# Kernel optimization log

Hardware: AMD Instinct MI355X
Metric: run time of the kernel (lower is better)

The kernel has to match this reference:

```python
import jax, jax.numpy as jnp
import numpy as np

D_MODEL = 512
NUM_HEADS = 8
HEAD_DIM = D_MODEL // NUM_HEADS
MAX_REL = 2


def setup_inputs() -> dict:
    key = jax.random.key(0)
    ks = jax.random.split(key, 12)
    B, S = 2, 4096
    std = 1.0 / np.sqrt(D_MODEL)
    inp = {
        'q': jax.random.normal(ks[0], (B, S, D_MODEL), jnp.float32),
        'k': jax.random.normal(ks[1], (B, S, D_MODEL), jnp.float32),
        'v': jax.random.normal(ks[2], (B, S, D_MODEL), jnp.float32),
        'Wq': jax.random.normal(ks[3], (D_MODEL, D_MODEL), jnp.float32) * std,
        'bq': jnp.zeros((D_MODEL,), jnp.float32),
        'Wk': jax.random.normal(ks[4], (D_MODEL, D_MODEL), jnp.float32) * std,
        'bk': jnp.zeros((D_MODEL,), jnp.float32),
        'Wv': jax.random.normal(ks[5], (D_MODEL, D_MODEL), jnp.float32) * std,
        'bv': jnp.zeros((D_MODEL,), jnp.float32),
        'Wo': jax.random.normal(ks[6], (D_MODEL, D_MODEL), jnp.float32) * std,
        'bo': jnp.zeros((D_MODEL,), jnp.float32),
        'rel_pos': jax.random.normal(ks[7], (NUM_HEADS, 2 * MAX_REL + 1), jnp.float32),
    }
    return inp


def _rel_bias(rel_pos, seq_len):
    pos = jnp.arange(seq_len)
    rel = pos[None, :] - pos[:, None]              # [S,S]
    idx = jnp.clip(rel, -MAX_REL, MAX_REL) + MAX_REL
    return rel_pos[:, idx]                         # [H,S,S]


def reference(q, k, v, Wq, bq, Wk, bk, Wv, bv, Wo, bo, rel_pos):
    B, S, D = q.shape
    H, Hd = NUM_HEADS, HEAD_DIM
    # torch Linear: x @ W.T + b
    Q = (q @ Wq.T + bq).reshape(B, S, H, Hd).transpose(0, 2, 1, 3)  # [B,H,S,Hd]
    K = (k @ Wk.T + bk).reshape(B, S, H, Hd).transpose(0, 2, 1, 3)
    V = (v @ Wv.T + bv).reshape(B, S, H, Hd).transpose(0, 2, 1, 3)
    scores = jnp.einsum('bhqd,bhkd->bhqk', Q, K) / jnp.sqrt(jnp.float32(Hd))
    scores = scores + _rel_bias(rel_pos, S)[None]                  # [B,H,S,S]
    probs = jax.nn.softmax(scores, axis=-1)
    attn = jnp.einsum('bhqk,bhkd->bhqd', probs, V)                 # [B,H,S,Hd]
    attn = attn.transpose(0, 2, 1, 3).reshape(B, S, D)
    return attn @ Wo.T + bo
```

## Files before the change

### kernel.cpp

```cpp
#include <hip/hip_runtime.h>

typedef __bf16 bf16_t;
typedef __bf16 bf16x4 __attribute__((ext_vector_type(4)));
typedef __bf16 bf16x8 __attribute__((ext_vector_type(8)));
typedef float f32x4 __attribute__((ext_vector_type(4)));

#define MFMA16(a, b, c) __builtin_amdgcn_mfma_f32_16x16x32_bf16(a, b, c, 0, 0, 0)
#define LOG2E 1.4426950408889634f
#define SHIFT 16.0f

#define GLL(g, l)                                                      \
  __builtin_amdgcn_global_load_lds(                                    \
      (const __attribute__((address_space(1))) void*)(g),              \
      (__attribute__((address_space(3))) void*)(l), 16, 0, 0)

static constexpr int NB = 2;
static constexpr int SEQ = 4096;
static constexpr int DM = 512;
static constexpr int NH = 8;
static constexpr int HD = 64;
static constexpr int M_ROWS = NB * SEQ;

__global__ __launch_bounds__(256) void cvt_w_kernel(
    const float* __restrict__ w0, const float* __restrict__ w1,
    const float* __restrict__ w2, const float* __restrict__ w3,
    bf16_t* __restrict__ out) {
  const float* src = (blockIdx.y == 0) ? w0 : (blockIdx.y == 1) ? w1
                   : (blockIdx.y == 2) ? w2 : w3;
  int i = (blockIdx.x * 256 + threadIdx.x) * 4;
  float4 v = *(const float4*)(src + i);
  bf16_t* o = out + blockIdx.y * (DM * DM) + i;
  o[0] = (bf16_t)v.x; o[1] = (bf16_t)v.y; o[2] = (bf16_t)v.z; o[3] = (bf16_t)v.w;
}

template <int XMODE>
__device__ __forceinline__ void gemm_body64(
    const void* __restrict__ Xv, const bf16_t* __restrict__ Wm,
    const float* __restrict__ bias, void* __restrict__ Out,
    int omode, float scale) {
  __shared__ bf16_t Asm[2][64 * 64];
  __shared__ bf16_t Bsm[2][128 * 64];

  const int tid = threadIdx.x;
  const int w = tid >> 6;
  const int lane = tid & 63;
  const int quad = lane >> 4, l15 = lane & 15;
  const int l8 = lane >> 3;
  const int swcol = ((lane & 7) ^ (l8 & 7)) * 8;
  const int m0 = blockIdx.x * 64;
  const int n0 = blockIdx.y * 128;
  const int moff = (w & 1) * 32;
  const int noff = (w >> 1) * 64;

  const bf16_t* Xb = (const bf16_t*)Xv;
  const float* Xf = (const float*)Xv;

  const int arow = tid >> 2;
  const int aseg = (tid & 3) * 16;
  const int ach = (tid & 3) * 2;
  const int asw = arow & 7;

  f32x4 acc[2][4];
#pragma unroll
  for (int mb = 0; mb < 2; mb++)
#pragma unroll
    for (int nb = 0; nb < 4; nb++) { acc[mb][nb][0] = 0.f; acc[mb][nb][1] = 0.f; acc[mb][nb][2] = 0.f; acc[mb][nb][3] = 0.f; }

#pragma unroll
  for (int j = 0; j < 4; j++) {
    const int row = j * 32 + w * 8 + l8;
    GLL(Wm + (size_t)(n0 + row) * DM + swcol, &Bsm[0][(j * 256 + w * 64) * 8]);
  }
  if (XMODE == 1) {
#pragma unroll
    for (int j = 0; j < 2; j++) {
      const int row = j * 32 + w * 8 + l8;
      GLL(Xb + (size_t)(m0 + row) * DM + swcol, &Asm[0][(j * 256 + w * 64) * 8]);
    }
  } else {
    const float* src = Xf + (size_t)(m0 + arow) * DM + aseg;
    float4 x0 = *(const float4*)(src);
    float4 x1 = *(const float4*)(src + 4);
    float4 x2 = *(const float4*)(src + 8);
    float4 x3 = *(const float4*)(src + 12);
    bf16x8 p0, p1;
    p0[0] = (bf16_t)x0.x; p0[1] = (bf16_t)x0.y; p0[2] = (bf16_t)x0.z; p0[3] = (bf16_t)x0.w;
    p0[4] = (bf16_t)x1.x; p0[5] = (bf16_t)x1.y; p0[6] = (bf16_t)x1.z; p0[7] = (bf16_t)x1.w;
    p1[0] = (bf16_t)x2.x; p1[1] = (bf16_t)x2.y; p1[2] = (bf16_t)x2.z; p1[3] = (bf16_t)x2.w;
    p1[4] = (bf16_t)x3.x; p1[5] = (bf16_t)x3.y; p1[6] = (bf16_t)x3.z; p1[7] = (bf16_t)x3.w;
    *(bf16x8*)&Asm[0][arow * 64 + ((ach ^ asw) * 8)] = p0;
    *(bf16x8*)&Asm[0][arow * 64 + (((ach + 1) ^ asw) * 8)] = p1;
  }
  __syncthreads();

  for (int ks = 0; ks < 8; ks++) {
    const int p = ks & 1, pn = p ^ 1;
    float4 xr0, xr1, xr2, xr3;
    if (ks < 7) {
      const int k0n = (ks + 1) * 64;
      if (XMODE == 0) {
        const float* src = Xf + (size_t)(m0 + arow) * DM + k0n + aseg;
        xr0 = *(const float4*)(src);
        xr1 = *(const float4*)(src + 4);
        xr2 = *(const float4*)(src + 8);
        xr3 = *(const float4*)(src + 12);
      } else {
#pragma unroll
        for (int j = 0; j < 2; j++) {
          const int row = j * 32 + w * 8 + l8;
          GLL(Xb + (size_t)(m0 + row) * DM + k0n + swcol,
              &Asm[pn][(j * 256 + w * 64) * 8]);
        }
      }
#pragma unroll
      for (int j = 0; j < 4; j++) {
        const int row = j * 32 + w * 8 + l8;
        GLL(Wm + (size_t)(n0 + row) * DM + k0n + swcol,
            &Bsm[pn][(j * 256 + w * 64) * 8]);
      }
    }

#pragma unroll
    for (int kd = 0; kd < 2; kd++) {
      const int fch = (((kd << 2) + quad) ^ (l15 & 7)) << 3;
      bf16x8 bfr[4];
#pragma unroll
      for (int nb = 0; nb < 4; nb++)
        bfr[nb] = *(const bf16x8*)&Bsm[p][(noff + nb * 16 + l15) * 64 + fch];
#pragma unroll
      for (int mb = 0; mb < 2; mb++) {
        bf16x8 a = *(const bf16x8*)&Asm[p][(moff + mb * 16 + l15) * 64 + fch];
#pragma unroll
        for (int nb = 0; nb < 4; nb++) acc[mb][nb] = MFMA16(a, bfr[nb], acc[mb][nb]);
      }
    }

    if (XMODE == 0 && ks < 7) {
      bf16x8 p0, p1;
      p0[0] = (bf16_t)xr0.x; p0[1] = (bf16_t)xr0.y; p0[2] = (bf16_t)xr0.z; p0[3] = (bf16_t)xr0.w;
      p0[4] = (bf16_t)xr1.x; p0[5] = (bf16_t)xr1.y; p0[6] = (bf16_t)xr1.z; p0[7] = (bf16_t)xr1.w;
      p1[0] = (bf16_t)xr2.x; p1[1] = (bf16_t)xr2.y; p1[2] = (bf16_t)xr2.z; p1[3] = (bf16_t)xr2.w;
      p1[4] = (bf16_t)xr3.x; p1[5] = (bf16_t)xr3.y; p1[6] = (bf16_t)xr3.z; p1[7] = (bf16_t)xr3.w;
      *(bf16x8*)&Asm[pn][arow * 64 + ((ach ^ asw) * 8)] = p0;
      *(bf16x8*)&Asm[pn][arow * 64 + (((ach + 1) ^ asw) * 8)] = p1;
    }
    __syncthreads();
  }

#pragma unroll
  for (int nb = 0; nb < 4; nb++) {
    const int n = n0 + noff + nb * 16 + l15;
    const float bn = bias[n];
    const int h = n >> 6, dd = n & 63;
#pragma unroll
    for (int mb = 0; mb < 2; mb++) {
      const int mbase = m0 + moff + mb * 16 + quad * 4;
      const int bb = mbase >> 12, s = mbase & 4095;
      if (omode == 0) {
#pragma unroll
        for (int r = 0; r < 4; r++) {
          const float val = (acc[mb][nb][r] + bn) * scale;
          ((bf16_t*)Out)[(size_t)((bb * NH + h) * SEQ + s + r) * HD + dd] = (bf16_t)val;
        }
      } else if (omode == 1) {
        bf16x4 pk;
#pragma unroll
        for (int r = 0; r < 4; r++) pk[r] = (bf16_t)(acc[mb][nb][r] + bn);
        *(bf16x4*)&((bf16_t*)Out)[(((size_t)(bb * NH + h) * HD + dd) << 12) + s] = pk;
      } else {
#pragma unroll
        for (int r = 0; r < 4; r++)
          ((float*)Out)[(size_t)(mbase + r) * DM + n] = acc[mb][nb][r] + bn;
      }
    }
  }
}

__global__ __launch_bounds__(256, 3) void qkv_kernel(
    const float* __restrict__ q, const float* __restrict__ k,
    const float* __restrict__ v, const bf16_t* __restrict__ Wall,
    const float* __restrict__ bq, const float* __restrict__ bk,
    const float* __restrict__ bv, bf16_t* __restrict__ Qb,
    bf16_t* __restrict__ Kb, bf16_t* __restrict__ Vb, float qscale) {
  const int z = blockIdx.z;
  const float* X = (z == 0) ? q : (z == 1) ? k : v;
  const float* bias = (z == 0) ? bq : (z == 1) ? bk : bv;
  bf16_t* Out = (z == 0) ? Qb : (z == 1) ? Kb : Vb;
  gemm_body64<0>(X, Wall + (size_t)z * DM * DM, bias, Out,
                 (z == 2) ? 1 : 0, (z == 0) ? qscale : 1.0f);
}

__global__ __launch_bounds__(256, 3) void oproj_kernel(
    const bf16_t* __restrict__ X, const bf16_t* __restrict__ Wm,
    const float* __restrict__ bias, float* __restrict__ Out) {
  gemm_body64<1>(X, Wm, bias, Out, 2, 1.0f);
}

__global__ __launch_bounds__(256, 2) void attn_kernel(
    const bf16_t* __restrict__ Qb, const bf16_t* __restrict__ Kb,
    const bf16_t* __restrict__ Vb, const float* __restrict__ rel_pos,
    bf16_t* __restrict__ attn_out) {
  __shared__ bf16_t Kt[2][64 * 64];
  __shared__ bf16_t Vt[2][64 * 64];
  __shared__ bf16_t Pt[4][32 * 64];

  const int tid = threadIdx.x;
  const int w = tid >> 6;
  const int lane = tid & 63;
  const int quad = lane >> 4, l15 = lane & 15;
  const int bh = blockIdx.y;
  const int b = bh >> 3, h = bh & 7;
  const int qlo = blockIdx.x * 128 + w * 32;

  const float rb0 = rel_pos[h * 5 + 0] * LOG2E;
  const float rb1 = rel_pos[h * 5 + 1] * LOG2E;
  const float rb2 = rel_pos[h * 5 + 2] * LOG2E;
  const float rb3 = rel_pos[h * 5 + 3] * LOG2E;
  const float rb4 = rel_pos[h * 5 + 4] * LOG2E;

  bf16x8 qf[2][2];
#pragma unroll
  for (int mb = 0; mb < 2; mb++)
#pragma unroll
    for (int kd = 0; kd < 2; kd++)
      qf[mb][kd] = *(const bf16x8*)(Qb + (size_t)(bh * SEQ + qlo + mb * 16 + l15) * HD + kd * 32 + 8 * quad);

  f32x4 o[2][4];
#pragma unroll
  for (int mb = 0; mb < 2; mb++)
#pragma unroll
    for (int db = 0; db < 4; db++) { o[mb][db][0] = 0.f; o[mb][db][1] = 0.f; o[mb][db][2] = 0.f; o[mb][db][3] = 0.f; }
  f32x4 l4[2];
  l4[0][0] = 0.f; l4[0][1] = 0.f; l4[0][2] = 0.f; l4[0][3] = 0.f;
  l4[1][0] = 0.f; l4[1][1] = 0.f; l4[1][2] = 0.f; l4[1][3] = 0.f;

  bf16x8 ones;
#pragma unroll
  for (int i = 0; i < 8; i++) ones[i] = (bf16_t)1.0f;

  const int srow = (w << 4) + (lane >> 3);
  const int scol = (((lane & 7) ^ (lane >> 3)) << 3);
  const bf16_t* kg0 = Kb + ((size_t)(bh * SEQ + srow) << 6) + scol;
  const bf16_t* vg0 = Vb + (((size_t)(bh * HD + srow)) << 12) + scol;
  const int ldst = (w << 10);

  const int sw = l15 & 7;
  const int kfo0 = (l15 << 6) + ((quad ^ sw) << 3);
  const int kfo1 = (l15 << 6) + (((quad + 4) ^ sw) << 3);

  GLL(kg0, &Kt[0][ldst]);
  GLL(kg0 + (8 << 6), &Kt[0][ldst + 512]);
  GLL(vg0, &Vt[0][ldst]);
  GLL(vg0 + (8 << 12), &Vt[0][ldst + 512]);
  __syncthreads();

  for (int t = 0; t < 64; t++) {
    const int p = t & 1, pn = p ^ 1;
    const int kk0 = t * 64;

    const int tg = (t < 63) ? t + 1 : 63;
    GLL(kg0 + ((size_t)tg << 12), &Kt[pn][ldst]);
    GLL(kg0 + ((size_t)tg << 12) + (8 << 6), &Kt[pn][ldst + 512]);
    GLL(vg0 + (tg << 6), &Vt[pn][ldst]);
    GLL(vg0 + (tg << 6) + (8 << 12), &Vt[pn][ldst + 512]);

    float cini;
    bool nearband = false;
    if (kk0 >= qlo + 33) {
      cini = rb4 - SHIFT;
    } else if (kk0 + 63 <= qlo - 2) {
      cini = rb0 - SHIFT;
    } else {
      cini = -SHIFT;
      nearband = true;
    }

    f32x4 s[2][4];
#pragma unroll
    for (int mb = 0; mb < 2; mb++)
#pragma unroll
      for (int kb = 0; kb < 4; kb++) { s[mb][kb][0] = cini; s[mb][kb][1] = cini; s[mb][kb][2] = cini; s[mb][kb][3] = cini; }
#pragma unroll
    for (int kb = 0; kb < 4; kb++) {
      bf16x8 kA0 = *(const bf16x8*)&Kt[p][kfo0 + (kb << 10)];
      bf16x8 kA1 = *(const bf16x8*)&Kt[p][kfo1 + (kb << 10)];
      s[0][kb] = MFMA16(kA0, qf[0][0], s[0][kb]);
      s[0][kb] = MFMA16(kA1, qf[0][1], s[0][kb]);
      s[1][kb] = MFMA16(kA0, qf[1][0], s[1][kb]);
      s[1][kb] = MFMA16(kA1, qf[1][1], s[1][kb]);
    }

    if (nearband) {
#pragma unroll
      for (int mb = 0; mb < 2; mb++) {
        const int qg = qlo + mb * 16 + l15;
#pragma unroll
        for (int kb = 0; kb < 4; kb++)
#pragma unroll
          for (int r = 0; r < 4; r++) {
            int dl = kk0 + kb * 16 + quad * 4 + r - qg;
            float bias = dl <= -2 ? rb0
                       : (dl >= 2 ? rb4
                       : (dl == -1 ? rb1 : (dl == 0 ? rb2 : rb3)));
            s[mb][kb][r] += bias;
          }
      }
    }

#pragma unroll
    for (int mb = 0; mb < 2; mb++) {
      bf16_t* Pr = &Pt[w][(mb * 16 + l15) * 64];
#pragma unroll
      for (int kb = 0; kb < 4; kb++) {
        bf16x4 pk;
#pragma unroll
        for (int r = 0; r < 4; r++)
          pk[r] = (bf16_t)__builtin_amdgcn_exp2f(s[mb][kb][r]);
        *(bf16x4*)&Pr[(((kb * 2 + (quad >> 1)) ^ sw) << 3) + ((quad & 1) << 2)] = pk;
      }
    }

    bf16x8 pf[2][2];
#pragma unroll
    for (int mb = 0; mb < 2; mb++)
#pragma unroll
      for (int kc = 0; kc < 2; kc++)
        pf[mb][kc] = *(const bf16x8*)&Pt[w][(mb * 16 + l15) * 64 + ((((kc << 2) + quad) ^ sw) << 3)];

    l4[0] = MFMA16(ones, pf[0][0], l4[0]);
    l4[0] = MFMA16(ones, pf[0][1], l4[0]);
    l4[1] = MFMA16(ones, pf[1][0], l4[1]);
    l4[1] = MFMA16(ones, pf[1][1], l4[1]);

#pragma unroll
    for (int db = 0; db < 4; db++) {
      bf16x8 vA0 = *(const bf16x8*)&Vt[p][kfo0 + (db << 10)];
      bf16x8 vA1 = *(const bf16x8*)&Vt[p][kfo1 + (db << 10)];
      o[0][db] = MFMA16(vA0, pf[0][0], o[0][db]);
      o[0][db] = MFMA16(vA1, pf[0][1], o[0][db]);
      o[1][db] = MFMA16(vA0, pf[1][0], o[1][db]);
      o[1][db] = MFMA16(vA1, pf[1][1], o[1][db]);
    }

    __syncthreads();
  }

#pragma unroll
  for (int mb = 0; mb < 2; mb++) {
    const float inv = 1.0f / l4[mb][0];
    const int qg = qlo + mb * 16 + l15;
#pragma unroll
    for (int db = 0; db < 4; db++) {
      bf16x4 pk;
#pragma unroll
      for (int r = 0; r < 4; r++) pk[r] = (bf16_t)(o[mb][db][r] * inv);
      *(bf16x4*)(attn_out + (size_t)(b * SEQ + qg) * DM + h * HD + db * 16 + quad * 4) = pk;
    }
  }
}

extern "C" void kernel_launch(void* const* d_in, const int* in_sizes, int n_in,
                              void* d_out, int out_size, void* d_ws, size_t ws_size,
                              hipStream_t stream) {
  const float* q   = (const float*)d_in[0];
  const float* k   = (const float*)d_in[1];
  const float* v   = (const float*)d_in[2];
  const float* Wq  = (const float*)d_in[3];
  const float* bq  = (const float*)d_in[4];
  const float* Wk  = (const float*)d_in[5];
  const float* bk  = (const float*)d_in[6];
  const float* Wv  = (const float*)d_in[7];
  const float* bv  = (const float*)d_in[8];
  const float* Wo  = (const float*)d_in[9];
  const float* bo  = (const float*)d_in[10];
  const float* rel = (const float*)d_in[11];

  char* ws = (char*)d_ws;
  bf16_t* Wbf  = (bf16_t*)ws;
  bf16_t* Qbuf = (bf16_t*)(ws + (size_t)(2  << 20));
  bf16_t* Kbuf = (bf16_t*)(ws + (size_t)(10 << 20));
  bf16_t* Vbuf = (bf16_t*)(ws + (size_t)(18 << 20));
  bf16_t* Abuf = (bf16_t*)(ws + (size_t)(26 << 20));

  cvt_w_kernel<<<dim3(256, 4), 256, 0, stream>>>(Wq, Wk, Wv, Wo, Wbf);

  const float qscale = LOG2E / 8.0f;
  qkv_kernel<<<dim3(128, 4, 3), 256, 0, stream>>>(
      q, k, v, Wbf, bq, bk, bv, Qbuf, Kbuf, Vbuf, qscale);

  attn_kernel<<<dim3(32, 16), 256, 0, stream>>>(Qbuf, Kbuf, Vbuf, rel, Abuf);

  oproj_kernel<<<dim3(128, 4), 256, 0, stream>>>(Abuf, Wbf + 3 * DM * DM, bo, (float*)d_out);
}
```

Measured before the change: 240.8 us.

## Triple-buffer GEMM and attention tiles with one barrier; pre-convert inputs to bf16

Replaces the double-buffered LDS pipelines in the GEMM and attention kernels with a three-stage ring. Each iteration uses one vmcnt-limited wait plus barrier, so two tiles are in flight and the trailing __syncthreads is gone. Adds a separate kernel that converts q/k/v fp32 to bf16 up front, so the QKV GEMM can load X with direct global-to-LDS loads instead of register convert-and-store. The cost is an extra kernel launch, extra global traffic for the bf16 copies, more LDS per block (occupancy hint lowered from 3 to 2), and reuse of the X buffer region for the attention output.

Result: no change. 239.7 us (-0.5%).

```diff
diff --git a/kernel.cpp b/kernel.cpp
--- a/kernel.cpp
+++ b/kernel.cpp
@@ -13,6 +13,9 @@
   __builtin_amdgcn_global_load_lds(                                    \
       (const __attribute__((address_space(1))) void*)(g),              \
       (__attribute__((address_space(3))) void*)(l), 16, 0, 0)
+
+#define WAIT_BARRIER_V4() asm volatile("s_waitcnt vmcnt(4)\n\ts_barrier" ::: "memory")
+#define WAIT_BARRIER_V6() asm volatile("s_waitcnt vmcnt(6)\n\ts_barrier" ::: "memory")
 
 static constexpr int NB = 2;
 static constexpr int SEQ = 4096;
@@ -33,92 +36,66 @@
   o[0] = (bf16_t)v.x; o[1] = (bf16_t)v.y; o[2] = (bf16_t)v.z; o[3] = (bf16_t)v.w;
 }
 
-template <int XMODE>
+__global__ __launch_bounds__(256) void cvt_x_kernel(
+    const float* __restrict__ q, const float* __restrict__ k,
+    const float* __restrict__ v, bf16_t* __restrict__ out) {
+  const float* src = (blockIdx.y == 0) ? q : (blockIdx.y == 1) ? k : v;
+  bf16_t* dst = out + (size_t)blockIdx.y * (M_ROWS * DM);
+  int i = (blockIdx.x * 256 + threadIdx.x) * 8;
+  float4 a = *(const float4*)(src + i);
+  float4 b = *(const float4*)(src + i + 4);
+  bf16x8 o;
+  o[0] = (bf16_t)a.x; o[1] = (bf16_t)a.y; o[2] = (bf16_t)a.z; o[3] = (bf16_t)a.w;
+  o[4] = (bf16_t)b.x; o[5] = (bf16_t)b.y; o[6] = (bf16_t)b.z; o[7] = (bf16_t)b.w;
+  *(bf16x8*)(dst + i) = o;
+}
+
 __device__ __forceinline__ void gemm_body64(
-    const void* __restrict__ Xv, const bf16_t* __restrict__ Wm,
+    const bf16_t* __restrict__ X, const bf16_t* __restrict__ Wm,
     const float* __restrict__ bias, void* __restrict__ Out,
     int omode, float scale) {
-  __shared__ bf16_t Asm[2][64 * 64];
-  __shared__ bf16_t Bsm[2][128 * 64];
+  __shared__ bf16_t Asm[3][64 * 64];
+  __shared__ bf16_t Bsm[3][128 * 64];
 
   const int tid = threadIdx.x;
   const int w = tid >> 6;
   const int lane = tid & 63;
   const int quad = lane >> 4, l15 = lane & 15;
   const int l8 = lane >> 3;
-  const int swcol = ((lane & 7) ^ (l8 & 7)) * 8;
+  const int swcol = ((lane & 7) ^ l8) * 8;
   const int m0 = blockIdx.x * 64;
   const int n0 = blockIdx.y * 128;
   const int moff = (w & 1) * 32;
   const int noff = (w >> 1) * 64;
 
-  const bf16_t* Xb = (const bf16_t*)Xv;
-  const float* Xf = (const float*)Xv;
-
-  const int arow = tid >> 2;
-  const int aseg = (tid & 3) * 16;
-  const int ach = (tid & 3) * 2;
-  const int asw = arow & 7;
-
   f32x4 acc[2][4];
 #pragma unroll
   for (int mb = 0; mb < 2; mb++)
 #pragma unroll
     for (int nb = 0; nb < 4; nb++) { acc[mb][nb][0] = 0.f; acc[mb][nb][1] = 0.f; acc[mb][nb][2] = 0.f; acc[mb][nb][3] = 0.f; }
 
-#pragma unroll
-  for (int j = 0; j < 4; j++) {
-    const int row = j * 32 + w * 8 + l8;
-    GLL(Wm + (size_t)(n0 + row) * DM + swcol, &Bsm[0][(j * 256 + w * 64) * 8]);
-  }
-  if (XMODE == 1) {
+  auto stage = [&](int ks, int bufi) {
+    const int k0 = ks * 64;
+#pragma unroll
+    for (int j = 0; j < 4; j++) {
+      const int row = j * 32 + w * 8 + l8;
+      GLL(Wm + (size_t)(n0 + row) * DM + k0 + swcol, &Bsm[bufi][(j * 256 + w * 64) * 8]);
+    }
 #pragma unroll
     for (int j = 0; j < 2; j++) {
       const int row = j * 32 + w * 8 + l8;
-      GLL(Xb + (size_t)(m0 + row) * DM + swcol, &Asm[0][(j * 256 + w * 64) * 8]);
-    }
-  } else {
-    const float* src = Xf + (size_t)(m0 + arow) * DM + aseg;
-    float4 x0 = *(const float4*)(src);
-    float4 x1 = *(const float4*)(src + 4);
-    float4 x2 = *(const float4*)(src + 8);
-    float4 x3 = *(const float4*)(src + 12);
-    bf16x8 p0, p1;
-    p0[0] = (bf16_t)x0.x; p0[1] = (bf16_t)x0.y; p0[2] = (bf16_t)x0.z; p0[3] = (bf16_t)x0.w;
-    p0[4] = (bf16_t)x1.x; p0[5] = (bf16_t)x1.y; p0[6] = (bf16_t)x1.z; p0[7] = (bf16_t)x1.w;
-    p1[0] = (bf16_t)x2.x; p1[1] = (bf16_t)x2.y; p1[2] = (bf16_t)x2.z; p1[3] = (bf16_t)x2.w;
-    p1[4] = (bf16_t)x3.x; p1[5] = (bf16_t)x3.y; p1[6] = (bf16_t)x3.z; p1[7] = (bf16_t)x3.w;
-    *(bf16x8*)&Asm[0][arow * 64 + ((ach ^ asw) * 8)] = p0;
-    *(bf16x8*)&Asm[0][arow * 64 + (((ach + 1) ^ asw) * 8)] = p1;
-  }
-  __syncthreads();
+      GLL(X + (size_t)(m0 + row) * DM + k0 + swcol, &Asm[bufi][(j * 256 + w * 64) * 8]);
+    }
+  };
+
+  stage(0, 0);
+  stage(1, 1);
 
   for (int ks = 0; ks < 8; ks++) {
-    const int p = ks & 1, pn = p ^ 1;
-    float4 xr0, xr1, xr2, xr3;
-    if (ks < 7) {
-      const int k0n = (ks + 1) * 64;
-      if (XMODE == 0) {
-        const float* src = Xf + (size_t)(m0 + arow) * DM + k0n + aseg;
-        xr0 = *(const float4*)(src);
-        xr1 = *(const float4*)(src + 4);
-        xr2 = *(const float4*)(src + 8);
-        xr3 = *(const float4*)(src + 12);
-      } else {
-#pragma unroll
-        for (int j = 0; j < 2; j++) {
-          const int row = j * 32 + w * 8 + l8;
-          GLL(Xb + (size_t)(m0 + row) * DM + k0n + swcol,
-              &Asm[pn][(j * 256 + w * 64) * 8]);
-        }
-      }
-#pragma unroll
-      for (int j = 0; j < 4; j++) {
-        const int row = j * 32 + w * 8 + l8;
-        GLL(Wm + (size_t)(n0 + row) * DM + k0n + swcol,
-            &Bsm[pn][(j * 256 + w * 64) * 8]);
-      }
-    }
+    WAIT_BARRIER_V6();
+    const int tn = (ks + 2 < 8) ? ks + 2 : 7;
+    stage(tn, (ks + 2) % 3);
+    const int p = ks % 3;
 
 #pragma unroll
     for (int kd = 0; kd < 2; kd++) {
@@ -134,17 +111,6 @@
         for (int nb = 0; nb < 4; nb++) acc[mb][nb] = MFMA16(a, bfr[nb], acc[mb][nb]);
       }
     }
-
-    if (XMODE == 0 && ks < 7) {
-      bf16x8 p0, p1;
-      p0[0] = (bf16_t)xr0.x; p0[1] = (bf16_t)xr0.y; p0[2] = (bf16_t)xr0.z; p0[3] = (bf16_t)xr0.w;
-      p0[4] = (bf16_t)xr1.x; p0[5] = (bf16_t)xr1.y; p0[6] = (bf16_t)xr1.z; p0[7] = (bf16_t)xr1.w;
-      p1[0] = (bf16_t)xr2.x; p1[1] = (bf16_t)xr2.y; p1[2] = (bf16_t)xr2.z; p1[3] = (bf16_t)xr2.w;
-      p1[4] = (bf16_t)xr3.x; p1[5] = (bf16_t)xr3.y; p1[6] = (bf16_t)xr3.z; p1[7] = (bf16_t)xr3.w;
-      *(bf16x8*)&Asm[pn][arow * 64 + ((ach ^ asw) * 8)] = p0;
-      *(bf16x8*)&Asm[pn][arow * 64 + (((ach + 1) ^ asw) * 8)] = p1;
-    }
-    __syncthreads();
   }
 
 #pragma unroll
@@ -176,32 +142,31 @@
   }
 }
 
-__global__ __launch_bounds__(256, 3) void qkv_kernel(
-    const float* __restrict__ q, const float* __restrict__ k,
-    const float* __restrict__ v, const bf16_t* __restrict__ Wall,
+__global__ __launch_bounds__(256, 2) void qkv_kernel(
+    const bf16_t* __restrict__ Xall, const bf16_t* __restrict__ Wall,
     const float* __restrict__ bq, const float* __restrict__ bk,
     const float* __restrict__ bv, bf16_t* __restrict__ Qb,
     bf16_t* __restrict__ Kb, bf16_t* __restrict__ Vb, float qscale) {
   const int z = blockIdx.z;
-  const float* X = (z == 0) ? q : (z == 1) ? k : v;
+  const bf16_t* X = Xall + (size_t)z * (M_ROWS * DM);
   const float* bias = (z == 0) ? bq : (z == 1) ? bk : bv;
   bf16_t* Out = (z == 0) ? Qb : (z == 1) ? Kb : Vb;
-  gemm_body64<0>(X, Wall + (size_t)z * DM * DM, bias, Out,
-                 (z == 2) ? 1 : 0, (z == 0) ? qscale : 1.0f);
-}
-
-__global__ __launch_bounds__(256, 3) void oproj_kernel(
+  gemm_body64(X, Wall + (size_t)z * DM * DM, bias, Out,
+              (z == 2) ? 1 : 0, (z == 0) ? qscale : 1.0f);
+}
+
+__global__ __launch_bounds__(256, 2) void oproj_kernel(
     const bf16_t* __restrict__ X, const bf16_t* __restrict__ Wm,
     const float* __restrict__ bias, float* __restrict__ Out) {
-  gemm_body64<1>(X, Wm, bias, Out, 2, 1.0f);
+  gemm_body64(X, Wm, bias, Out, 2, 1.0f);
 }
 
 __global__ __launch_bounds__(256, 2) void attn_kernel(
     const bf16_t* __restrict__ Qb, const bf16_t* __restrict__ Kb,
     const bf16_t* __restrict__ Vb, const float* __restrict__ rel_pos,
     bf16_t* __restrict__ attn_out) {
-  __shared__ bf16_t Kt[2][64 * 64];
-  __shared__ bf16_t Vt[2][64 * 64];
+  __shared__ bf16_t Kt[3][64 * 64];
+  __shared__ bf16_t Vt[3][64 * 64];
   __shared__ bf16_t Pt[4][32 * 64];
 
   const int tid = threadIdx.x;
@@ -248,21 +213,22 @@
   const int kfo0 = (l15 << 6) + ((quad ^ sw) << 3);
   const int kfo1 = (l15 << 6) + (((quad + 4) ^ sw) << 3);
 
-  GLL(kg0, &Kt[0][ldst]);
-  GLL(kg0 + (8 << 6), &Kt[0][ldst + 512]);
-  GLL(vg0, &Vt[0][ldst]);
-  GLL(vg0 + (8 << 12), &Vt[0][ldst + 512]);
-  __syncthreads();
+  auto stage = [&](int t, int bufi) {
+    GLL(kg0 + ((size_t)t << 12), &Kt[bufi][ldst]);
+    GLL(kg0 + ((size_t)t << 12) + (8 << 6), &Kt[bufi][ldst + 512]);
+    GLL(vg0 + (t << 6), &Vt[bufi][ldst]);
+    GLL(vg0 + (t << 6) + (8 << 12), &Vt[bufi][ldst + 512]);
+  };
+
+  stage(0, 0);
+  stage(1, 1);
 
   for (int t = 0; t < 64; t++) {
-    const int p = t & 1, pn = p ^ 1;
+    WAIT_BARRIER_V4();
+    const int tg = (t + 2 < 64) ? t + 2 : 63;
+    stage(tg, (t + 2) % 3);
+    const int p = t % 3;
     const int kk0 = t * 64;
-
-    const int tg = (t < 63) ? t + 1 : 63;
-    GLL(kg0 + ((size_t)tg << 12), &Kt[pn][ldst]);
-    GLL(kg0 + ((size_t)tg << 12) + (8 << 6), &Kt[pn][ldst + 512]);
-    GLL(vg0 + (tg << 6), &Vt[pn][ldst]);
-    GLL(vg0 + (tg << 6) + (8 << 12), &Vt[pn][ldst + 512]);
 
     float cini;
     bool nearband = false;
@@ -341,8 +307,6 @@
       o[1][db] = MFMA16(vA0, pf[1][0], o[1][db]);
       o[1][db] = MFMA16(vA1, pf[1][1], o[1][db]);
     }
-
-    __syncthreads();
   }
 
 #pragma unroll
@@ -377,16 +341,18 @@
 
   char* ws = (char*)d_ws;
   bf16_t* Wbf  = (bf16_t*)ws;
-  bf16_t* Qbuf = (bf16_t*)(ws + (size_t)(2  << 20));
-  bf16_t* Kbuf = (bf16_t*)(ws + (size_t)(10 << 20));
-  bf16_t* Vbuf = (bf16_t*)(ws + (size_t)(18 << 20));
-  bf16_t* Abuf = (bf16_t*)(ws + (size_t)(26 << 20));
+  bf16_t* Xb   = (bf16_t*)(ws + (size_t)(2  << 20));
+  bf16_t* Qbuf = (bf16_t*)(ws + (size_t)(26 << 20));
+  bf16_t* Kbuf = (bf16_t*)(ws + (size_t)(34 << 20));
+  bf16_t* Vbuf = (bf16_t*)(ws + (size_t)(42 << 20));
+  bf16_t* Abuf = (bf16_t*)(ws + (size_t)(2  << 20));
 
   cvt_w_kernel<<<dim3(256, 4), 256, 0, stream>>>(Wq, Wk, Wv, Wo, Wbf);
+  cvt_x_kernel<<<dim3(2048, 3), 256, 0, stream>>>(q, k, v, Xb);
 
   const float qscale = LOG2E / 8.0f;
   qkv_kernel<<<dim3(128, 4, 3), 256, 0, stream>>>(
-      q, k, v, Wbf, bq, bk, bv, Qbuf, Kbuf, Vbuf, qscale);
+      Xb, Wbf, bq, bk, bv, Qbuf, Kbuf, Vbuf, qscale);
 
   attn_kernel<<<dim3(32, 16), 256, 0, stream>>>(Qbuf, Kbuf, Vbuf, rel, Abuf);
 
```
